# Kernel tuning notes

Measured on AMD Instinct MI355X. Metric: run time of the kernel, lower is better.

## Reference

```python
import jax, jax.numpy as jnp
import numpy as np

N_HEAD = 8
LN_EPS = 1e-6


def setup_inputs() -> dict:
    key = jax.random.key(0)
    ks = jax.random.split(key, 6)
    B, S, D = 4, 2048, 256  # D = hidden_size*2 = input_dim
    sc = 1.0 / np.sqrt(D)
    return {
        "inputs": jax.random.normal(ks[0], (B, S, D), jnp.float32),
        "Wq": jax.random.normal(ks[1], (D, D), jnp.float32) * sc,
        "Wk": jax.random.normal(ks[2], (D, D), jnp.float32) * sc,
        "Wv": jax.random.normal(ks[3], (D, D), jnp.float32) * sc,
        "Wf": jax.random.normal(ks[4], (D, D), jnp.float32) * sc,
        "bf": jnp.zeros((D,), jnp.float32),
        "gamma": jnp.ones((D,), jnp.float32),
        "beta": jnp.zeros((D,), jnp.float32),
    }


def reference(inputs, Wq, Wk, Wv, Wf, bf, gamma, beta):
    B, S, D = inputs.shape
    H = N_HEAD
    dh = D // H
    # Projections (torch Linear: x @ W.T), no bias for Q/K/V
    Q = (inputs @ Wq.T).reshape(B, S, H, dh)
    K = (inputs @ Wk.T).reshape(B, S, H, dh)
    V = (inputs @ Wv.T).reshape(B, S, H, dh)
    # NOTE: original scales by sqrt(K.shape[1]) == sqrt(seq_len), not sqrt(dh)
    scale = 1.0 / jnp.sqrt(jnp.float32(S)).astype(inputs.dtype)
    scores = jnp.einsum("bqhd,bkhd->bhqk", Q, K) * scale  # [B,H,S,S]
    attn = jax.nn.softmax(scores, axis=-1)
    out = jnp.einsum("bhqk,bkhd->bqhd", attn, V).reshape(B, S, D)
    out = out @ Wf.T + bf
    # residual + LayerNorm(eps=1e-6)
    x = inputs + out
    mu = jnp.mean(x, axis=-1, keepdims=True)
    var = jnp.mean(jnp.square(x - mu), axis=-1, keepdims=True)
    return (x - mu) * jax.lax.rsqrt(var + LN_EPS) * gamma + beta
```

## Files before the change

kernel.cpp:

```cpp
#include <hip/hip_runtime.h>
#include <hip/hip_bf16.h>

typedef __attribute__((ext_vector_type(8))) short short8;
typedef __attribute__((ext_vector_type(4))) float f32x4;
typedef __attribute__((ext_vector_type(16))) float f32x16;

#define DEVI __device__ __forceinline__

DEVI unsigned short f2bf(float f) {
  union { float f; unsigned int u; } v; v.f = f;
  unsigned int r = v.u + 0x7fffu + ((v.u >> 16) & 1u);
  return (unsigned short)(r >> 16);
}

#define SB 4
#define SS 2048
#define SD 256
#define SH 8
#define SDH 32
#define SM 8192

#define QSCALE 0.0318793654f

#define XBF_OFF 0
#define W_OFF   (SM * SD)
#define Q_OFF   (W_OFF + 4 * SD * SD)
#define K_OFF   (Q_OFF + SM * SD)
#define VT_OFF  (K_OFF + SM * SD)
#define AO_OFF  (VT_OFF + SM * SD)

__global__ __launch_bounds__(256) void convert_k(
    const float* __restrict__ X, const float* __restrict__ Wq,
    const float* __restrict__ Wk, const float* __restrict__ Wv,
    const float* __restrict__ Wf, unsigned short* __restrict__ ws) {
  const int XN = SM * SD;
  const int WN = SD * SD;
  int i4 = (blockIdx.x * 256 + threadIdx.x) * 4;
  const float* src; unsigned short* dst; int idx;
  if (i4 < XN)             { src = X;  dst = ws + XBF_OFF;      idx = i4; }
  else if (i4 < XN + WN)   { src = Wq; dst = ws + W_OFF;        idx = i4 - XN; }
  else if (i4 < XN + 2*WN) { src = Wk; dst = ws + W_OFF + WN;   idx = i4 - XN - WN; }
  else if (i4 < XN + 3*WN) { src = Wv; dst = ws + W_OFF + 2*WN; idx = i4 - XN - 2*WN; }
  else if (i4 < XN + 4*WN) { src = Wf; dst = ws + W_OFF + 3*WN; idx = i4 - XN - 3*WN; }
  else return;
  float4 v = *reinterpret_cast<const float4*>(src + idx);
  unsigned short o[4] = { f2bf(v.x), f2bf(v.y), f2bf(v.z), f2bf(v.w) };
  *reinterpret_cast<uint2*>(dst + idx) = *reinterpret_cast<const uint2*>(o);
}

__global__ __launch_bounds__(256) void qkv_k(const unsigned short* __restrict__ ws_c,
                                             unsigned short* __restrict__ ws) {
  __shared__ __align__(16) unsigned short Al[64][72];
  __shared__ __align__(16) unsigned short Bl[64][72];
  const unsigned short* Xb = ws_c + XBF_OFF;
  const unsigned short* W  = ws_c + W_OFF + blockIdx.z * (SD * SD);
  int tid = threadIdx.x;
  int w = tid >> 6, lane = tid & 63, g = lane >> 4, r = lane & 15;
  int m0 = blockIdx.x * 64, n0 = blockIdx.y * 64;
  f32x4 acc[4] = {};
  int srow = tid >> 3, scol = (tid & 7) * 8;
  for (int k0 = 0; k0 < SD; k0 += 64) {
    short8 a0 = *reinterpret_cast<const short8*>(Xb + (m0 + srow) * SD + k0 + scol);
    short8 a1 = *reinterpret_cast<const short8*>(Xb + (m0 + srow + 32) * SD + k0 + scol);
    short8 b0 = *reinterpret_cast<const short8*>(W + (n0 + srow) * SD + k0 + scol);
    short8 b1 = *reinterpret_cast<const short8*>(W + (n0 + srow + 32) * SD + k0 + scol);
    __syncthreads();
    *reinterpret_cast<short8*>(&Al[srow][scol]) = a0;
    *reinterpret_cast<short8*>(&Al[srow + 32][scol]) = a1;
    *reinterpret_cast<short8*>(&Bl[srow][scol]) = b0;
    *reinterpret_cast<short8*>(&Bl[srow + 32][scol]) = b1;
    __syncthreads();
#pragma unroll
    for (int ks = 0; ks < 2; ks++) {
      short8 af = *reinterpret_cast<const short8*>(&Al[w * 16 + r][ks * 32 + g * 8]);
#pragma unroll
      for (int nt = 0; nt < 4; nt++) {
        short8 bb = *reinterpret_cast<const short8*>(&Bl[nt * 16 + r][ks * 32 + g * 8]);
        acc[nt] = __builtin_amdgcn_mfma_f32_16x16x32_bf16(af, bb, acc[nt], 0, 0, 0);
      }
    }
  }
  int z = blockIdx.z;
  if (z < 2) {
    unsigned short* out = ws + (z == 0 ? Q_OFF : K_OFF);
    float qs = (z == 0) ? QSCALE : 1.0f;
#pragma unroll
    for (int nt = 0; nt < 4; nt++) {
      int n = n0 + nt * 16 + r;
      int h = n >> 5, d = n & 31;
#pragma unroll
      for (int j = 0; j < 4; j++) {
        int m = m0 + w * 16 + g * 4 + j;
        int b = m >> 11, s = m & 2047;
        out[(((b << 3) + h) * SS + s) * SDH + d] = f2bf(acc[nt][j] * qs);
      }
    }
  } else {
    unsigned short* out = ws + VT_OFF;
#pragma unroll
    for (int nt = 0; nt < 4; nt++) {
      int n = n0 + nt * 16 + r;
      int h = n >> 5, d = n & 31;
      int m = m0 + w * 16 + g * 4;
      int b = m >> 11, s = m & 2047;
      unsigned short o4[4];
#pragma unroll
      for (int j = 0; j < 4; j++) o4[j] = f2bf(acc[nt][j]);
      *reinterpret_cast<uint2*>(out + ((((b << 3) + h) << 5) + d) * SS + s) =
          *reinterpret_cast<const uint2*>(o4);
    }
  }
}

__global__ __launch_bounds__(256) void attn_k(const unsigned short* __restrict__ ws_c,
                                              unsigned short* __restrict__ ws) {
  __shared__ __align__(16) unsigned short Kl[64][40];
  __shared__ __align__(16) unsigned short Vl[32][72];
  __shared__ float Linv[4][32];
  int tid = threadIdx.x, w = tid >> 6, lane = tid & 63;
  int n32 = lane & 31, hi = lane >> 5;
  int wg = ((blockIdx.x & 7) << 6) + (blockIdx.x >> 3);
  int bh = wg >> 4, qb = wg & 15;
  int q0 = qb * 128 + w * 32;
  const unsigned short* Qh = ws_c + Q_OFF + bh * (SS * SDH);
  const unsigned short* Kh = ws_c + K_OFF + bh * (SS * SDH);
  const unsigned short* Vh = ws_c + VT_OFF + bh * (SDH * SS);
  short8 qB0 = *reinterpret_cast<const short8*>(Qh + (q0 + n32) * SDH + 8 * hi);
  short8 qB1 = *reinterpret_cast<const short8*>(Qh + (q0 + n32) * SDH + 16 + 8 * hi);
  int krow = tid >> 2, kcol = (tid & 3) * 8;
  int vrow = tid >> 3, vcol = (tid & 7) * 8;
  f32x16 O = {};
  float Lacc = 0.f;
  short8 kst = *reinterpret_cast<const short8*>(Kh + krow * SDH + kcol);
  short8 vst = *reinterpret_cast<const short8*>(Vh + vrow * SS + vcol);
  for (int t = 0; t < 32; ++t) {
    __syncthreads();
    *reinterpret_cast<short8*>(&Kl[krow][kcol]) = kst;
    *reinterpret_cast<short8*>(&Vl[vrow][vcol]) = vst;
    __syncthreads();
    if (t < 31) {
      kst = *reinterpret_cast<const short8*>(Kh + ((t + 1) * 64 + krow) * SDH + kcol);
      vst = *reinterpret_cast<const short8*>(Vh + vrow * SS + (t + 1) * 64 + vcol);
    }
#pragma unroll
    for (int sub = 0; sub < 2; ++sub) {
      short8 kA0 = *reinterpret_cast<const short8*>(&Kl[sub * 32 + n32][8 * hi]);
      short8 kA1 = *reinterpret_cast<const short8*>(&Kl[sub * 32 + n32][16 + 8 * hi]);
      short8 vB0 = *reinterpret_cast<const short8*>(&Vl[n32][sub * 32 + 8 * hi]);
      short8 vB1 = *reinterpret_cast<const short8*>(&Vl[n32][sub * 32 + 16 + 8 * hi]);
      f32x16 acc = {};
      acc = __builtin_amdgcn_mfma_f32_32x32x16_bf16(kA0, qB0, acc, 0, 0, 0);
      acc = __builtin_amdgcn_mfma_f32_32x32x16_bf16(kA1, qB1, acc, 0, 0, 0);
      float p[16];
#pragma unroll
      for (int i = 0; i < 16; ++i) p[i] = __builtin_amdgcn_exp2f(acc[i]);
      float s0 = 0.f, s1 = 0.f;
#pragma unroll
      for (int i = 0; i < 8; ++i) { s0 += p[2 * i]; s1 += p[2 * i + 1]; }
      Lacc += s0 + s1;
      unsigned int pk[8];
#pragma unroll
      for (int i = 0; i < 8; ++i) {
        unsigned int rr;
        asm("v_cvt_pk_bf16_f32 %0, %1, %2" : "=v"(rr) : "v"(p[2 * i]), "v"(p[2 * i + 1]));
        pk[i] = rr;
      }
      asm("v_permlane32_swap_b32 %0, %1" : "+v"(pk[0]), "+v"(pk[2]));
      asm("v_permlane32_swap_b32 %0, %1" : "+v"(pk[1]), "+v"(pk[3]));
      asm("v_permlane32_swap_b32 %0, %1" : "+v"(pk[4]), "+v"(pk[6]));
      asm("v_permlane32_swap_b32 %0, %1" : "+v"(pk[5]), "+v"(pk[7]));
      union { unsigned int u[4]; short8 s; } A1, A2;
      A1.u[0] = pk[0]; A1.u[1] = pk[1]; A1.u[2] = pk[2]; A1.u[3] = pk[3];
      A2.u[0] = pk[4]; A2.u[1] = pk[5]; A2.u[2] = pk[6]; A2.u[3] = pk[7];
      O = __builtin_amdgcn_mfma_f32_32x32x16_bf16(A1.s, vB0, O, 0, 0, 0);
      O = __builtin_amdgcn_mfma_f32_32x32x16_bf16(A2.s, vB1, O, 0, 0, 0);
    }
  }
  float Lt = Lacc + __shfl_xor(Lacc, 32);
  if (lane < 32) Linv[w][n32] = 1.0f / Lt;
  __syncthreads();
  int b = bh >> 3, h = bh & 7;
  unsigned short* AO = ws + AO_OFF;
#pragma unroll
  for (int r = 0; r < 16; ++r) {
    int q = (r & 3) + 8 * (r >> 2) + 4 * hi;
    AO[(b * SS + q0 + q) * SD + h * SDH + n32] = f2bf(O[r] * Linv[w][q]);
  }
}

__global__ __launch_bounds__(256) void final_k(
    const unsigned short* __restrict__ ws_c, const float* __restrict__ X,
    const float* __restrict__ bfv, const float* __restrict__ gamma,
    const float* __restrict__ beta, float* __restrict__ out) {
  __shared__ __align__(16) unsigned short Al[32][72];
  __shared__ __align__(16) unsigned short Bl[256][72];
  __shared__ float Cl[32][257];
  const unsigned short* AO = ws_c + AO_OFF;
  const unsigned short* Wf = ws_c + W_OFF + 3 * (SD * SD);
  int tid = threadIdx.x, w = tid >> 6, lane = tid & 63, g = lane >> 4, r = lane & 15;
  int m0 = blockIdx.x * 32;
  f32x4 acc[2][4] = {};
  int arow = tid >> 3, acol = (tid & 7) * 8;
  for (int k0 = 0; k0 < SD; k0 += 64) {
    short8 av = *reinterpret_cast<const short8*>(AO + (m0 + arow) * SD + k0 + acol);
    short8 bv[8];
#pragma unroll
    for (int i = 0; i < 8; i++)
      bv[i] = *reinterpret_cast<const short8*>(Wf + (i * 32 + arow) * SD + k0 + acol);
    __syncthreads();
    *reinterpret_cast<short8*>(&Al[arow][acol]) = av;
#pragma unroll
    for (int i = 0; i < 8; i++)
      *reinterpret_cast<short8*>(&Bl[i * 32 + arow][acol]) = bv[i];
    __syncthreads();
#pragma unroll
    for (int ks = 0; ks < 2; ks++) {
      short8 af0 = *reinterpret_cast<const short8*>(&Al[r][ks * 32 + g * 8]);
      short8 af1 = *reinterpret_cast<const short8*>(&Al[16 + r][ks * 32 + g * 8]);
#pragma unroll
      for (int nt = 0; nt < 4; nt++) {
        short8 bb = *reinterpret_cast<const short8*>(&Bl[w * 64 + nt * 16 + r][ks * 32 + g * 8]);
        acc[0][nt] = __builtin_amdgcn_mfma_f32_16x16x32_bf16(af0, bb, acc[0][nt], 0, 0, 0);
        acc[1][nt] = __builtin_amdgcn_mfma_f32_16x16x32_bf16(af1, bb, acc[1][nt], 0, 0, 0);
      }
    }
  }
#pragma unroll
  for (int rt = 0; rt < 2; rt++)
#pragma unroll
    for (int nt = 0; nt < 4; nt++)
#pragma unroll
      for (int j = 0; j < 4; j++)
        Cl[rt * 16 + g * 4 + j][w * 64 + nt * 16 + r] = acc[rt][nt][j];
  __syncthreads();
  int row = tid >> 3, sub = tid & 7;
  int m = m0 + row;
  float x[32];
  float sum = 0.f, sumsq = 0.f;
#pragma unroll
  for (int i = 0; i < 8; i++) {
    int col = sub * 32 + i * 4;
    float4 xv = *reinterpret_cast<const float4*>(X + m * SD + col);
    float4 bb = *reinterpret_cast<const float4*>(bfv + col);
    x[i * 4 + 0] = Cl[row][col + 0] + xv.x + bb.x;
    x[i * 4 + 1] = Cl[row][col + 1] + xv.y + bb.y;
    x[i * 4 + 2] = Cl[row][col + 2] + xv.z + bb.z;
    x[i * 4 + 3] = Cl[row][col + 3] + xv.w + bb.w;
  }
#pragma unroll
  for (int c = 0; c < 32; c++) { sum += x[c]; sumsq += x[c] * x[c]; }
  sum += __shfl_xor(sum, 1);  sumsq += __shfl_xor(sumsq, 1);
  sum += __shfl_xor(sum, 2);  sumsq += __shfl_xor(sumsq, 2);
  sum += __shfl_xor(sum, 4);  sumsq += __shfl_xor(sumsq, 4);
  float mean = sum * (1.0f / 256.0f);
  float var = sumsq * (1.0f / 256.0f) - mean * mean;
  float rstd = rsqrtf(var + 1e-6f);
#pragma unroll
  for (int i = 0; i < 8; i++) {
    int col = sub * 32 + i * 4;
    float4 gv = *reinterpret_cast<const float4*>(gamma + col);
    float4 bv2 = *reinterpret_cast<const float4*>(beta + col);
    float4 ov;
    ov.x = (x[i * 4 + 0] - mean) * rstd * gv.x + bv2.x;
    ov.y = (x[i * 4 + 1] - mean) * rstd * gv.y + bv2.y;
    ov.z = (x[i * 4 + 2] - mean) * rstd * gv.z + bv2.z;
    ov.w = (x[i * 4 + 3] - mean) * rstd * gv.w + bv2.w;
    *reinterpret_cast<float4*>(out + m * SD + col) = ov;
  }
}

extern "C" void kernel_launch(void* const* d_in, const int* in_sizes, int n_in,
                              void* d_out, int out_size, void* d_ws, size_t ws_size,
                              hipStream_t stream) {
  const float* X  = (const float*)d_in[0];
  const float* Wq = (const float*)d_in[1];
  const float* Wk = (const float*)d_in[2];
  const float* Wv = (const float*)d_in[3];
  const float* Wf = (const float*)d_in[4];
  const float* bf = (const float*)d_in[5];
  const float* gm = (const float*)d_in[6];
  const float* bt = (const float*)d_in[7];
  float* out = (float*)d_out;
  unsigned short* ws = (unsigned short*)d_ws;

  convert_k<<<2304, 256, 0, stream>>>(X, Wq, Wk, Wv, Wf, ws);
  qkv_k<<<dim3(128, 4, 3), 256, 0, stream>>>(ws, ws);
  attn_k<<<dim3(512), 256, 0, stream>>>(ws, ws);
  final_k<<<256, 256, 0, stream>>>(ws, X, bf, gm, bt, out);
}
```

Baseline: 66.87 us.

## Split attention KV range across two wave groups and enlarge QKV GEMM tiles

```diff
diff --git a/kernel.cpp b/kernel.cpp
--- a/kernel.cpp
+++ b/kernel.cpp
@@ -50,107 +50,135 @@
 
 __global__ __launch_bounds__(256) void qkv_k(const unsigned short* __restrict__ ws_c,
                                              unsigned short* __restrict__ ws) {
-  __shared__ __align__(16) unsigned short Al[64][72];
-  __shared__ __align__(16) unsigned short Bl[64][72];
+  __shared__ __align__(16) unsigned short Atile[128][72];
+  __shared__ __align__(16) unsigned short Btile[128][72];
   const unsigned short* Xb = ws_c + XBF_OFF;
-  const unsigned short* W  = ws_c + W_OFF + blockIdx.z * (SD * SD);
-  int tid = threadIdx.x;
-  int w = tid >> 6, lane = tid & 63, g = lane >> 4, r = lane & 15;
-  int m0 = blockIdx.x * 64, n0 = blockIdx.y * 64;
-  f32x4 acc[4] = {};
+  const unsigned short* Wall = ws_c + W_OFF;
+  int tid = threadIdx.x, w = tid >> 6, lane = tid & 63, g = lane >> 4, r = lane & 15;
+  int m0 = blockIdx.x * 128, n0 = blockIdx.y * 128;
+  int wr = (w >> 1) * 64, wc = (w & 1) * 64;
+  f32x4 acc[4][4] = {};
   int srow = tid >> 3, scol = (tid & 7) * 8;
   for (int k0 = 0; k0 < SD; k0 += 64) {
-    short8 a0 = *reinterpret_cast<const short8*>(Xb + (m0 + srow) * SD + k0 + scol);
-    short8 a1 = *reinterpret_cast<const short8*>(Xb + (m0 + srow + 32) * SD + k0 + scol);
-    short8 b0 = *reinterpret_cast<const short8*>(W + (n0 + srow) * SD + k0 + scol);
-    short8 b1 = *reinterpret_cast<const short8*>(W + (n0 + srow + 32) * SD + k0 + scol);
-    __syncthreads();
-    *reinterpret_cast<short8*>(&Al[srow][scol]) = a0;
-    *reinterpret_cast<short8*>(&Al[srow + 32][scol]) = a1;
-    *reinterpret_cast<short8*>(&Bl[srow][scol]) = b0;
-    *reinterpret_cast<short8*>(&Bl[srow + 32][scol]) = b1;
-    __syncthreads();
-#pragma unroll
-    for (int ks = 0; ks < 2; ks++) {
-      short8 af = *reinterpret_cast<const short8*>(&Al[w * 16 + r][ks * 32 + g * 8]);
-#pragma unroll
-      for (int nt = 0; nt < 4; nt++) {
-        short8 bb = *reinterpret_cast<const short8*>(&Bl[nt * 16 + r][ks * 32 + g * 8]);
-        acc[nt] = __builtin_amdgcn_mfma_f32_16x16x32_bf16(af, bb, acc[nt], 0, 0, 0);
-      }
-    }
-  }
-  int z = blockIdx.z;
+    short8 a[4], b[4];
+#pragma unroll
+    for (int p = 0; p < 4; ++p) {
+      a[p] = *reinterpret_cast<const short8*>(Xb + (m0 + srow + p * 32) * SD + k0 + scol);
+      b[p] = *reinterpret_cast<const short8*>(Wall + (n0 + srow + p * 32) * SD + k0 + scol);
+    }
+    __syncthreads();
+#pragma unroll
+    for (int p = 0; p < 4; ++p) {
+      *reinterpret_cast<short8*>(&Atile[srow + p * 32][scol]) = a[p];
+      *reinterpret_cast<short8*>(&Btile[srow + p * 32][scol]) = b[p];
+    }
+    __syncthreads();
+#pragma unroll
+    for (int ks = 0; ks < 2; ++ks) {
+      short8 af[4], bf[4];
+#pragma unroll
+      for (int i = 0; i < 4; ++i)
+        af[i] = *reinterpret_cast<const short8*>(&Atile[wr + i * 16 + r][ks * 32 + g * 8]);
+#pragma unroll
+      for (int j = 0; j < 4; ++j)
+        bf[j] = *reinterpret_cast<const short8*>(&Btile[wc + j * 16 + r][ks * 32 + g * 8]);
+#pragma unroll
+      for (int i = 0; i < 4; ++i)
+#pragma unroll
+        for (int j = 0; j < 4; ++j)
+          acc[i][j] = __builtin_amdgcn_mfma_f32_16x16x32_bf16(af[i], bf[j], acc[i][j], 0, 0, 0);
+    }
+  }
+  int z = n0 >> 8;
+  int nbase = n0 & 255;
   if (z < 2) {
     unsigned short* out = ws + (z == 0 ? Q_OFF : K_OFF);
     float qs = (z == 0) ? QSCALE : 1.0f;
 #pragma unroll
-    for (int nt = 0; nt < 4; nt++) {
-      int n = n0 + nt * 16 + r;
-      int h = n >> 5, d = n & 31;
-#pragma unroll
-      for (int j = 0; j < 4; j++) {
-        int m = m0 + w * 16 + g * 4 + j;
-        int b = m >> 11, s = m & 2047;
-        out[(((b << 3) + h) * SS + s) * SDH + d] = f2bf(acc[nt][j] * qs);
+    for (int j = 0; j < 4; ++j) {
+      int col = nbase + wc + j * 16 + r;
+      int h = col >> 5, d = col & 31;
+#pragma unroll
+      for (int i = 0; i < 4; ++i) {
+#pragma unroll
+        for (int jj = 0; jj < 4; ++jj) {
+          int m = m0 + wr + i * 16 + g * 4 + jj;
+          int b_ = m >> 11, s = m & 2047;
+          out[(((b_ << 3) + h) * SS + s) * SDH + d] = f2bf(acc[i][j][jj] * qs);
+        }
       }
     }
   } else {
     unsigned short* out = ws + VT_OFF;
 #pragma unroll
-    for (int nt = 0; nt < 4; nt++) {
-      int n = n0 + nt * 16 + r;
-      int h = n >> 5, d = n & 31;
-      int m = m0 + w * 16 + g * 4;
-      int b = m >> 11, s = m & 2047;
-      unsigned short o4[4];
-#pragma unroll
-      for (int j = 0; j < 4; j++) o4[j] = f2bf(acc[nt][j]);
-      *reinterpret_cast<uint2*>(out + ((((b << 3) + h) << 5) + d) * SS + s) =
-          *reinterpret_cast<const uint2*>(o4);
-    }
-  }
-}
-
-__global__ __launch_bounds__(256) void attn_k(const unsigned short* __restrict__ ws_c,
-                                              unsigned short* __restrict__ ws) {
-  __shared__ __align__(16) unsigned short Kl[64][40];
-  __shared__ __align__(16) unsigned short Vl[32][72];
+    for (int j = 0; j < 4; ++j) {
+      int col = nbase + wc + j * 16 + r;
+      int h = col >> 5, d = col & 31;
+#pragma unroll
+      for (int i = 0; i < 4; ++i) {
+        int m = m0 + wr + i * 16 + g * 4;
+        int b_ = m >> 11, s = m & 2047;
+        unsigned short o4[4];
+#pragma unroll
+        for (int jj = 0; jj < 4; ++jj) o4[jj] = f2bf(acc[i][j][jj]);
+        *reinterpret_cast<uint2*>(out + ((((b_ << 3) + h) << 5) + d) * SS + s) =
+            *reinterpret_cast<const uint2*>(o4);
+      }
+    }
+  }
+}
+
+#define TKV 128
+__global__ __launch_bounds__(512, 4) void attn_k(const unsigned short* __restrict__ ws_c,
+                                                 unsigned short* __restrict__ ws) {
+  __shared__ __align__(16) unsigned short Kl[2][TKV][40];
+  __shared__ __align__(16) unsigned short Vl[2][32][TKV + 8];
+  __shared__ float OC[4][64][16];
+  __shared__ float LC[4][64];
   __shared__ float Linv[4][32];
   int tid = threadIdx.x, w = tid >> 6, lane = tid & 63;
+  int wg = w >> 2, wl = w & 3, gtid = tid & 255;
   int n32 = lane & 31, hi = lane >> 5;
-  int wg = ((blockIdx.x & 7) << 6) + (blockIdx.x >> 3);
-  int bh = wg >> 4, qb = wg & 15;
-  int q0 = qb * 128 + w * 32;
+  int wgid = ((blockIdx.x & 7) << 6) + (blockIdx.x >> 3);
+  int bh = wgid >> 4, qb = wgid & 15;
+  int q0 = qb * 128 + wl * 32;
   const unsigned short* Qh = ws_c + Q_OFF + bh * (SS * SDH);
-  const unsigned short* Kh = ws_c + K_OFF + bh * (SS * SDH);
-  const unsigned short* Vh = ws_c + VT_OFF + bh * (SDH * SS);
+  const unsigned short* Kg = ws_c + K_OFF + bh * (SS * SDH) + wg * 1024 * SDH;
+  const unsigned short* Vg = ws_c + VT_OFF + bh * (SDH * SS) + wg * 1024;
   short8 qB0 = *reinterpret_cast<const short8*>(Qh + (q0 + n32) * SDH + 8 * hi);
   short8 qB1 = *reinterpret_cast<const short8*>(Qh + (q0 + n32) * SDH + 16 + 8 * hi);
-  int krow = tid >> 2, kcol = (tid & 3) * 8;
-  int vrow = tid >> 3, vcol = (tid & 7) * 8;
+  int krow = gtid >> 2, kcol = (gtid & 3) * 8;
+  int vrow = gtid >> 4, vcol = (gtid & 15) * 8;
   f32x16 O = {};
   float Lacc = 0.f;
-  short8 kst = *reinterpret_cast<const short8*>(Kh + krow * SDH + kcol);
-  short8 vst = *reinterpret_cast<const short8*>(Vh + vrow * SS + vcol);
-  for (int t = 0; t < 32; ++t) {
-    __syncthreads();
-    *reinterpret_cast<short8*>(&Kl[krow][kcol]) = kst;
-    *reinterpret_cast<short8*>(&Vl[vrow][vcol]) = vst;
-    __syncthreads();
-    if (t < 31) {
-      kst = *reinterpret_cast<const short8*>(Kh + ((t + 1) * 64 + krow) * SDH + kcol);
-      vst = *reinterpret_cast<const short8*>(Vh + vrow * SS + (t + 1) * 64 + vcol);
-    }
-#pragma unroll
-    for (int sub = 0; sub < 2; ++sub) {
-      short8 kA0 = *reinterpret_cast<const short8*>(&Kl[sub * 32 + n32][8 * hi]);
-      short8 kA1 = *reinterpret_cast<const short8*>(&Kl[sub * 32 + n32][16 + 8 * hi]);
-      short8 vB0 = *reinterpret_cast<const short8*>(&Vl[n32][sub * 32 + 8 * hi]);
-      short8 vB1 = *reinterpret_cast<const short8*>(&Vl[n32][sub * 32 + 16 + 8 * hi]);
+  short8 ka = *reinterpret_cast<const short8*>(Kg + krow * SDH + kcol);
+  short8 kb = *reinterpret_cast<const short8*>(Kg + (64 + krow) * SDH + kcol);
+  short8 va = *reinterpret_cast<const short8*>(Vg + vrow * SS + vcol);
+  short8 vb = *reinterpret_cast<const short8*>(Vg + (16 + vrow) * SS + vcol);
+  for (int t = 0; t < 8; ++t) {
+    __syncthreads();
+    *reinterpret_cast<short8*>(&Kl[wg][krow][kcol]) = ka;
+    *reinterpret_cast<short8*>(&Kl[wg][64 + krow][kcol]) = kb;
+    *reinterpret_cast<short8*>(&Vl[wg][vrow][vcol]) = va;
+    *reinterpret_cast<short8*>(&Vl[wg][16 + vrow][vcol]) = vb;
+    __syncthreads();
+    if (t < 7) {
+      ka = *reinterpret_cast<const short8*>(Kg + ((t + 1) * TKV + krow) * SDH + kcol);
+      kb = *reinterpret_cast<const short8*>(Kg + ((t + 1) * TKV + 64 + krow) * SDH + kcol);
+      va = *reinterpret_cast<const short8*>(Vg + vrow * SS + (t + 1) * TKV + vcol);
+      vb = *reinterpret_cast<const short8*>(Vg + (16 + vrow) * SS + (t + 1) * TKV + vcol);
+    }
+#pragma unroll
+    for (int s = 0; s < 4; ++s) {
+      short8 kA0 = *reinterpret_cast<const short8*>(&Kl[wg][s * 32 + n32][8 * hi]);
+      short8 kA1 = *reinterpret_cast<const short8*>(&Kl[wg][s * 32 + n32][16 + 8 * hi]);
+      short8 vB0 = *reinterpret_cast<const short8*>(&Vl[wg][n32][s * 32 + 8 * hi]);
+      short8 vB1 = *reinterpret_cast<const short8*>(&Vl[wg][n32][s * 32 + 16 + 8 * hi]);
       f32x16 acc = {};
+      __builtin_amdgcn_s_setprio(1);
       acc = __builtin_amdgcn_mfma_f32_32x32x16_bf16(kA0, qB0, acc, 0, 0, 0);
       acc = __builtin_amdgcn_mfma_f32_32x32x16_bf16(kA1, qB1, acc, 0, 0, 0);
+      __builtin_amdgcn_s_setprio(0);
       float p[16];
 #pragma unroll
       for (int i = 0; i < 16; ++i) p[i] = __builtin_amdgcn_exp2f(acc[i]);
@@ -169,22 +197,34 @@
       asm("v_permlane32_swap_b32 %0, %1" : "+v"(pk[1]), "+v"(pk[3]));
       asm("v_permlane32_swap_b32 %0, %1" : "+v"(pk[4]), "+v"(pk[6]));
       asm("v_permlane32_swap_b32 %0, %1" : "+v"(pk[5]), "+v"(pk[7]));
-      union { unsigned int u[4]; short8 s; } A1, A2;
+      union { unsigned int u[4]; short8 sv; } A1, A2;
       A1.u[0] = pk[0]; A1.u[1] = pk[1]; A1.u[2] = pk[2]; A1.u[3] = pk[3];
       A2.u[0] = pk[4]; A2.u[1] = pk[5]; A2.u[2] = pk[6]; A2.u[3] = pk[7];
-      O = __builtin_amdgcn_mfma_f32_32x32x16_bf16(A1.s, vB0, O, 0, 0, 0);
-      O = __builtin_amdgcn_mfma_f32_32x32x16_bf16(A2.s, vB1, O, 0, 0, 0);
-    }
-  }
-  float Lt = Lacc + __shfl_xor(Lacc, 32);
-  if (lane < 32) Linv[w][n32] = 1.0f / Lt;
+      __builtin_amdgcn_s_setprio(1);
+      O = __builtin_amdgcn_mfma_f32_32x32x16_bf16(A1.sv, vB0, O, 0, 0, 0);
+      O = __builtin_amdgcn_mfma_f32_32x32x16_bf16(A2.sv, vB1, O, 0, 0, 0);
+      __builtin_amdgcn_s_setprio(0);
+    }
+  }
+  if (wg == 1) {
+#pragma unroll
+    for (int i = 0; i < 16; ++i) OC[wl][lane][i] = O[i];
+    LC[wl][lane] = Lacc;
+  }
   __syncthreads();
-  int b = bh >> 3, h = bh & 7;
-  unsigned short* AO = ws + AO_OFF;
-#pragma unroll
-  for (int r = 0; r < 16; ++r) {
-    int q = (r & 3) + 8 * (r >> 2) + 4 * hi;
-    AO[(b * SS + q0 + q) * SD + h * SDH + n32] = f2bf(O[r] * Linv[w][q]);
+  if (wg == 0) {
+#pragma unroll
+    for (int i = 0; i < 16; ++i) O[i] += OC[wl][lane][i];
+    Lacc += LC[wl][lane];
+    float Lt = Lacc + __shfl_xor(Lacc, 32);
+    if (lane < 32) Linv[wl][n32] = 1.0f / Lt;
+    int b = bh >> 3, h = bh & 7;
+    unsigned short* AO = ws + AO_OFF;
+#pragma unroll
+    for (int rr = 0; rr < 16; ++rr) {
+      int q = (rr & 3) + 8 * (rr >> 2) + 4 * hi;
+      AO[(b * SS + q0 + q) * SD + h * SDH + n32] = f2bf(O[rr] * Linv[wl][q]);
+    }
   }
 }
 
@@ -284,7 +324,7 @@
   unsigned short* ws = (unsigned short*)d_ws;
 
   convert_k<<<2304, 256, 0, stream>>>(X, Wq, Wk, Wv, Wf, ws);
-  qkv_k<<<dim3(128, 4, 3), 256, 0, stream>>>(ws, ws);
-  attn_k<<<dim3(512), 256, 0, stream>>>(ws, ws);
+  qkv_k<<<dim3(64, 6), 256, 0, stream>>>(ws, ws);
+  attn_k<<<dim3(512), 512, 0, stream>>>(ws, ws);
   final_k<<<256, 256, 0, stream>>>(ws, X, bf, gm, bt, out);
 }
```

Result: faster. 60.23 us (-9.9%).
